# Kernel optimization log

Measured on AMD Instinct MI355X. Metric: run time of the kernel, lower is better.

Reference implementation:

```python
import jax, jax.numpy as jnp
import numpy as np

L = 4      # num_gnn_layers
D = 128    # dim_latent
N = 50000  # nodes
E = 800000 # edges
BN_EPS = 1e-5


def setup_inputs() -> dict:
    key = jax.random.key(0)
    ks = jax.random.split(key, 16)
    w = lambda k: jax.random.normal(k, (L, D, D), jnp.float32) * 0.05
    b = lambda k: jax.random.normal(k, (L, D), jnp.float32) * 0.05
    return {
        "edge_index": jax.random.randint(ks[0], (2, E), 0, N, dtype=jnp.int64),
        "h": jax.random.normal(ks[1], (N, D), jnp.float32),
        "e": jax.random.normal(ks[2], (E, D), jnp.float32),
        "WA": w(ks[3]), "bA": b(ks[4]),
        "WB": w(ks[5]), "bB": b(ks[6]),
        "WC": w(ks[7]), "bC": b(ks[8]),
        "WU": w(ks[9]), "bU": b(ks[10]),
        "WVf": w(ks[11]), "bVf": b(ks[12]),
        "WVb": w(ks[13]), "bVb": b(ks[14]),
        "bnh_g": jnp.ones((L, D), jnp.float32), "bnh_b": jnp.zeros((L, D), jnp.float32),
        "bne_g": jnp.ones((L, D), jnp.float32), "bne_b": jnp.zeros((L, D), jnp.float32),
    }


def _bn(x, g, b):
    # BatchNorm1d, track_running_stats=False -> batch stats, biased variance
    mu = jnp.mean(x, axis=0)
    var = jnp.mean(jnp.square(x - mu), axis=0)
    return (x - mu) * jax.lax.rsqrt(var + BN_EPS) * g + b


def reference(edge_index, h, e,
              WA, bA, WB, bB, WC, bC, WU, bU, WVf, bVf, WVb, bVb,
              bnh_g, bnh_b, bne_g, bne_b):
    n = h.shape[0]
    s0, s1 = edge_index[0], edge_index[1]  # propagate always uses s0 -> s1

    for l in range(L):
        A = h @ WA[l].T + bA[l]
        B = h @ WB[l].T + bB[l]
        C = e @ WC[l].T + bC[l]
        U = h @ WU[l].T + bU[l]
        Vf = h @ WVf[l].T + bVf[l]
        Vb = h @ WVb[l].T + bVb[l]

        def gate(V, gsrc, gdst):
            ne = A[gsrc] + B[gdst] + C                      # [E, D]
            ne = jax.nn.relu(_bn(ne, bne_g[l], bne_b[l])) + e
            sig = jax.nn.sigmoid(ne)
            msg = V[s0] * sig / (sig + 1e-6)                # [E, D]
            agg = jax.ops.segment_sum(msg, s1, num_segments=n)
            return agg, ne

        h_f, e_f = gate(Vf, s0, s1)   # forward gate
        h_b, _ = gate(Vb, s1, s0)     # backward gate (A/B roles swapped only)

        h_new = jax.nn.relu(_bn(h_f + h_b + U, bnh_g[l], bnh_b[l])) + h
        h, e = h_new, e_f             # dropout is identity in eval

    return h, e
```

## Files before the change

kernel.cpp:

```cpp
#include <hip/hip_runtime.h>
#include <hip/hip_bf16.h>

#define N_NODES 50000
#define N_EDGES 800000
#define DIM 128
#define NLAYERS 4
#define BN_EPS 1e-5f
#define ECH 64

typedef unsigned short bf16_t;
typedef __attribute__((ext_vector_type(8))) short bf16x8;
typedef __attribute__((ext_vector_type(4))) float f32x4;

__device__ __forceinline__ float bf2f(bf16_t x) {
    unsigned int u = ((unsigned int)x) << 16;
    return __uint_as_float(u);
}
__device__ __forceinline__ bf16_t f2bf(float f) {
    unsigned int u = __float_as_uint(f);
    unsigned int r = (u + 0x7FFFu + ((u >> 16) & 1u)) >> 16;
    return (bf16_t)r;
}

__global__ __launch_bounds__(128) void node_gemm(
    const float* __restrict__ h,
    const float* __restrict__ WA, const float* __restrict__ bA,
    const float* __restrict__ WB, const float* __restrict__ bB,
    const float* __restrict__ WU, const float* __restrict__ bU,
    const float* __restrict__ WVf, const float* __restrict__ bVf,
    const float* __restrict__ WVb, const float* __restrict__ bVb,
    bf16_t* __restrict__ A, bf16_t* __restrict__ B, bf16_t* __restrict__ U,
    bf16_t* __restrict__ Vf, bf16_t* __restrict__ Vb)
{
    __shared__ float hl[8][DIM];
    const int t = threadIdx.x;
    const long n0 = (long)blockIdx.x * 8;
    #pragma unroll
    for (int i = 0; i < 8; ++i) hl[i][t] = h[(n0 + i) * DIM + t];
    __syncthreads();

    const float* Ws[5] = {WA, WB, WU, WVf, WVb};
    const float* bs[5] = {bA, bB, bU, bVf, bVb};
    float acc[5][8];
    #pragma unroll
    for (int m = 0; m < 5; ++m) {
        float bv = bs[m][t];
        #pragma unroll
        for (int n = 0; n < 8; ++n) acc[m][n] = bv;
    }
    const float4* wr[5];
    #pragma unroll
    for (int m = 0; m < 5; ++m) wr[m] = (const float4*)(Ws[m] + (size_t)t * DIM);

    #pragma unroll 4
    for (int j4 = 0; j4 < DIM / 4; ++j4) {
        float4 h4[8];
        #pragma unroll
        for (int n = 0; n < 8; ++n) h4[n] = ((const float4*)hl[n])[j4];
        #pragma unroll
        for (int m = 0; m < 5; ++m) {
            float4 w = wr[m][j4];
            #pragma unroll
            for (int n = 0; n < 8; ++n)
                acc[m][n] += w.x * h4[n].x + w.y * h4[n].y + w.z * h4[n].z + w.w * h4[n].w;
        }
    }
    bf16_t* Os[5] = {A, B, U, Vf, Vb};
    #pragma unroll
    for (int m = 0; m < 5; ++m)
        #pragma unroll
        for (int n = 0; n < 8; ++n)
            Os[m][(n0 + n) * DIM + t] = f2bf(acc[m][n]);
}

#define EG_TILE 64
#define EG_TILES 5
#define EG_GRID (N_EDGES / (EG_TILE * EG_TILES))

__global__ __launch_bounds__(256) void edge_gemm_mfma(
    const float* __restrict__ e, const float* __restrict__ WC,
    const float* __restrict__ bC, bf16_t* __restrict__ C)
{
    __shared__ __align__(16) char elds[2][EG_TILE * 256];

    const int tid  = threadIdx.x;
    const int lane = tid & 63;
    const int wv   = tid >> 6;
    const int l16  = lane & 15;
    const int lk   = lane >> 4;

    bf16x8 bfrag[2][4];
    float bias[2];
    #pragma unroll
    for (int nt = 0; nt < 2; ++nt) {
        const int n = wv * 32 + nt * 16 + l16;
        bias[nt] = bC[n];
        #pragma unroll
        for (int ks = 0; ks < 4; ++ks) {
            const int k = ks * 32 + lk * 8;
            const float4* wp = (const float4*)(WC + (size_t)n * DIM + k);
            float4 w0 = wp[0], w1 = wp[1];
            union { bf16x8 v; bf16_t s[8]; } u;
            u.s[0] = f2bf(w0.x); u.s[1] = f2bf(w0.y);
            u.s[2] = f2bf(w0.z); u.s[3] = f2bf(w0.w);
            u.s[4] = f2bf(w1.x); u.s[5] = f2bf(w1.y);
            u.s[6] = f2bf(w1.z); u.s[7] = f2bf(w1.w);
            bfrag[nt][ks] = u.v;
        }
    }

    float4 sreg[4][2];
    const long tile0 = (long)blockIdx.x * EG_TILES;

    auto load_tile = [&](long tile) {
        #pragma unroll
        for (int j = 0; j < 4; ++j) {
            const int idx = j * 256 + tid;
            const int row = idx >> 4, cb = idx & 15;
            const float4* gp = (const float4*)(
                e + (size_t)(tile * EG_TILE + row) * DIM + cb * 8);
            sreg[j][0] = gp[0]; sreg[j][1] = gp[1];
        }
    };
    auto write_lds = [&](int buf) {
        #pragma unroll
        for (int j = 0; j < 4; ++j) {
            const int idx = j * 256 + tid;
            const int row = idx >> 4, cb = idx & 15;
            union { bf16x8 v; bf16_t s[8]; } u;
            float4 a = sreg[j][0], b = sreg[j][1];
            u.s[0] = f2bf(a.x); u.s[1] = f2bf(a.y);
            u.s[2] = f2bf(a.z); u.s[3] = f2bf(a.w);
            u.s[4] = f2bf(b.x); u.s[5] = f2bf(b.y);
            u.s[6] = f2bf(b.z); u.s[7] = f2bf(b.w);
            const int off = row * 256 + ((cb * 16) ^ ((row & 7) << 4));
            *(bf16x8*)(&elds[buf][off]) = u.v;
        }
    };

    load_tile(tile0);
    write_lds(0);
    __syncthreads();
    int cur = 0;

    for (int t = 0; t < EG_TILES; ++t) {
        if (t + 1 < EG_TILES) load_tile(tile0 + t + 1);

        f32x4 acc[4][2];
        #pragma unroll
        for (int mt = 0; mt < 4; ++mt)
            #pragma unroll
            for (int nt = 0; nt < 2; ++nt)
                acc[mt][nt] = (f32x4){0.f, 0.f, 0.f, 0.f};

        #pragma unroll
        for (int ks = 0; ks < 4; ++ks) {
            bf16x8 afrag[4];
            #pragma unroll
            for (int mt = 0; mt < 4; ++mt) {
                const int row = mt * 16 + l16;
                const int off = row * 256 +
                    ((ks * 64 + lk * 16) ^ ((row & 7) << 4));
                afrag[mt] = *(const bf16x8*)(&elds[cur][off]);
            }
            #pragma unroll
            for (int mt = 0; mt < 4; ++mt)
                #pragma unroll
                for (int nt = 0; nt < 2; ++nt)
                    acc[mt][nt] = __builtin_amdgcn_mfma_f32_16x16x32_bf16(
                        afrag[mt], bfrag[nt][ks], acc[mt][nt], 0, 0, 0);
        }

        const long e0 = (tile0 + t) * EG_TILE;
        #pragma unroll
        for (int mt = 0; mt < 4; ++mt) {
            const long rbase = e0 + mt * 16 + lk * 4;
            #pragma unroll
            for (int nt = 0; nt < 2; ++nt) {
                const int col = wv * 32 + nt * 16 + l16;
                #pragma unroll
                for (int r = 0; r < 4; ++r)
                    C[(rbase + r) * DIM + col] = f2bf(acc[mt][nt][r] + bias[nt]);
            }
        }

        if (t + 1 < EG_TILES) {
            write_lds(cur ^ 1);
            __syncthreads();
            cur ^= 1;
        }
    }
}

__global__ __launch_bounds__(128) void edge_stats(
    const int* __restrict__ s0, const int* __restrict__ s1,
    const bf16_t* __restrict__ A, const bf16_t* __restrict__ B,
    const bf16_t* __restrict__ C, float* __restrict__ stats)
{
    __shared__ int ls0[ECH], ls1[ECH];
    const int t = threadIdx.x;
    const long k0 = (long)blockIdx.x * ECH;
    if (t < ECH) { ls0[t] = s0[k0 + t]; ls1[t] = s1[k0 + t]; }
    __syncthreads();

    float sf = 0.f, ssf = 0.f, sb = 0.f, ssb = 0.f;
    for (int i = 0; i < ECH; ++i) {
        const long k = k0 + i;
        const long a = ls0[i], b = ls1[i];
        float c  = bf2f(C[k * DIM + t]);
        float a0 = bf2f(A[a * DIM + t]);
        float b1 = bf2f(B[b * DIM + t]);
        float a1 = bf2f(A[b * DIM + t]);
        float b0 = bf2f(B[a * DIM + t]);
        float tf = a0 + b1 + c;
        float tb = a1 + b0 + c;
        sf += tf; ssf += tf * tf;
        sb += tb; ssb += tb * tb;
    }
    atomicAdd(&stats[t], sf);
    atomicAdd(&stats[128 + t], ssf);
    atomicAdd(&stats[256 + t], sb);
    atomicAdd(&stats[384 + t], ssb);
}

__global__ void finalize_edge_stats(float* __restrict__ stats)
{
    const int t = threadIdx.x;
    const float inv = 1.0f / (float)N_EDGES;
    if (t < 128) {
        float mu = stats[t] * inv;
        float var = stats[128 + t] * inv - mu * mu;
        stats[768 + t] = mu;
        stats[896 + t] = rsqrtf(var + BN_EPS);
    } else {
        int d = t - 128;
        float mu = stats[256 + d] * inv;
        float var = stats[384 + d] * inv - mu * mu;
        stats[1024 + d] = mu;
        stats[1152 + d] = rsqrtf(var + BN_EPS);
    }
}

__global__ __launch_bounds__(128) void edge_apply(
    const int* __restrict__ s0, const int* __restrict__ s1,
    const bf16_t* __restrict__ A, const bf16_t* __restrict__ B,
    const bf16_t* __restrict__ C,
    const bf16_t* __restrict__ Vf, const bf16_t* __restrict__ Vb,
    const float* __restrict__ stats,
    const float* __restrict__ gne, const float* __restrict__ bne,
    float* __restrict__ ebuf, float* __restrict__ agg)
{
    __shared__ int ls0[ECH], ls1[ECH];
    const int t = threadIdx.x;
    const long k0 = (long)blockIdx.x * ECH;
    if (t < ECH) { ls0[t] = s0[k0 + t]; ls1[t] = s1[k0 + t]; }
    __syncthreads();

    const float g = gne[t], bb = bne[t];
    const float af = stats[896 + t] * g;
    const float cf = bb - stats[768 + t] * af;
    const float ab = stats[1152 + t] * g;
    const float cb = bb - stats[1024 + t] * ab;

    for (int i = 0; i < ECH; ++i) {
        const long k = k0 + i;
        const long sa = ls0[i], sd = ls1[i];
        float c  = bf2f(C[k * DIM + t]);
        float a0 = bf2f(A[sa * DIM + t]);
        float b1 = bf2f(B[sd * DIM + t]);
        float a1 = bf2f(A[sd * DIM + t]);
        float b0 = bf2f(B[sa * DIM + t]);
        float ek = ebuf[k * DIM + t];

        float nf = fmaxf((a0 + b1 + c) * af + cf, 0.0f) + ek;
        float nb = fmaxf((a1 + b0 + c) * ab + cb, 0.0f) + ek;
        ebuf[k * DIM + t] = nf;

        float sigf = 1.0f / (1.0f + __expf(-nf));
        float sigb = 1.0f / (1.0f + __expf(-nb));
        float wf = sigf / (sigf + 1e-6f);
        float wb = sigb / (sigb + 1e-6f);
        float msg = bf2f(Vf[sa * DIM + t]) * wf + bf2f(Vb[sa * DIM + t]) * wb;
        atomicAdd(&agg[sd * DIM + t], msg);
    }
}

__global__ __launch_bounds__(128) void node_stats(
    const float* __restrict__ agg, const bf16_t* __restrict__ U,
    float* __restrict__ stats)
{
    const int t = threadIdx.x;
    const long n0 = (long)blockIdx.x * 50;
    float s = 0.f, ss = 0.f;
    for (int i = 0; i < 50; ++i) {
        const long n = n0 + i;
        float v = agg[n * DIM + t] + bf2f(U[n * DIM + t]);
        s += v; ss += v * v;
    }
    atomicAdd(&stats[512 + t], s);
    atomicAdd(&stats[640 + t], ss);
}

__global__ void finalize_node_stats(float* __restrict__ stats)
{
    const int t = threadIdx.x;
    const float inv = 1.0f / (float)N_NODES;
    float mu = stats[512 + t] * inv;
    float var = stats[640 + t] * inv - mu * mu;
    stats[1280 + t] = mu;
    stats[1408 + t] = rsqrtf(var + BN_EPS);
}

__global__ __launch_bounds__(256) void node_apply(
    const float* __restrict__ agg, const bf16_t* __restrict__ U,
    const float* __restrict__ stats,
    const float* __restrict__ gh, const float* __restrict__ bh,
    float* __restrict__ hbuf)
{
    const long i = (long)blockIdx.x * 256 + threadIdx.x;
    const int d = (int)(i & (DIM - 1));
    float v = agg[i] + bf2f(U[i]);
    float n = (v - stats[1280 + d]) * stats[1408 + d] * gh[d] + bh[d];
    hbuf[i] = fmaxf(n, 0.0f) + hbuf[i];
}

extern "C" void kernel_launch(void* const* d_in, const int* in_sizes, int n_in,
                              void* d_out, int out_size, void* d_ws, size_t ws_size,
                              hipStream_t stream)
{
    const int* ei = (const int*)d_in[0];
    const int* s0 = ei;
    const int* s1 = ei + N_EDGES;
    const float* h0 = (const float*)d_in[1];
    const float* e0 = (const float*)d_in[2];
    const float* WA = (const float*)d_in[3];  const float* bA = (const float*)d_in[4];
    const float* WB = (const float*)d_in[5];  const float* bB = (const float*)d_in[6];
    const float* WC = (const float*)d_in[7];  const float* bC = (const float*)d_in[8];
    const float* WU = (const float*)d_in[9];  const float* bU = (const float*)d_in[10];
    const float* WVf = (const float*)d_in[11]; const float* bVf = (const float*)d_in[12];
    const float* WVb = (const float*)d_in[13]; const float* bVb = (const float*)d_in[14];
    const float* bnh_g = (const float*)d_in[15]; const float* bnh_b = (const float*)d_in[16];
    const float* bne_g = (const float*)d_in[17]; const float* bne_b = (const float*)d_in[18];

    float* hbuf = (float*)d_out;
    float* ebuf = hbuf + (size_t)N_NODES * DIM;

    float* agg = (float*)d_ws;
    float* stats = agg + (size_t)N_NODES * DIM;
    bf16_t* Abuf  = (bf16_t*)(stats + 2048);
    bf16_t* Bbuf  = Abuf  + (size_t)N_NODES * DIM;
    bf16_t* Ubuf  = Bbuf  + (size_t)N_NODES * DIM;
    bf16_t* Vfbuf = Ubuf  + (size_t)N_NODES * DIM;
    bf16_t* Vbbuf = Vfbuf + (size_t)N_NODES * DIM;
    bf16_t* Cbuf  = Vbbuf + (size_t)N_NODES * DIM;

    hipMemcpyAsync(hbuf, h0, (size_t)N_NODES * DIM * sizeof(float),
                   hipMemcpyDeviceToDevice, stream);
    hipMemcpyAsync(ebuf, e0, (size_t)N_EDGES * DIM * sizeof(float),
                   hipMemcpyDeviceToDevice, stream);

    for (int l = 0; l < NLAYERS; ++l) {
        const size_t wo = (size_t)l * DIM * DIM;
        const size_t bo = (size_t)l * DIM;
        hipMemsetAsync(agg, 0, ((size_t)N_NODES * DIM + 768) * sizeof(float), stream);

        node_gemm<<<N_NODES / 8, 128, 0, stream>>>(
            hbuf, WA + wo, bA + bo, WB + wo, bB + bo, WU + wo, bU + bo,
            WVf + wo, bVf + bo, WVb + wo, bVb + bo,
            Abuf, Bbuf, Ubuf, Vfbuf, Vbbuf);
        edge_gemm_mfma<<<EG_GRID, 256, 0, stream>>>(ebuf, WC + wo, bC + bo, Cbuf);
        edge_stats<<<N_EDGES / ECH, 128, 0, stream>>>(s0, s1, Abuf, Bbuf, Cbuf, stats);
        finalize_edge_stats<<<1, 256, 0, stream>>>(stats);
        edge_apply<<<N_EDGES / ECH, 128, 0, stream>>>(
            s0, s1, Abuf, Bbuf, Cbuf, Vfbuf, Vbbuf, stats,
            bne_g + bo, bne_b + bo, ebuf, agg);
        node_stats<<<N_NODES / 50, 128, 0, stream>>>(agg, Ubuf, stats);
        finalize_node_stats<<<1, 128, 0, stream>>>(stats);
        node_apply<<<(N_NODES * DIM) / 256, 256, 0, stream>>>(
            agg, Ubuf, stats, bnh_g + bo, bnh_b + bo, hbuf);
    }
}
```

Before: 5.499 ms.

## Use MFMA for node GEMM and destination-sorted edge apply with run-merged atomics

Replaces the scalar FP32 node GEMM with a bf16 MFMA kernel that converts h and the weights to bf16 on the fly. It also adds a one-time counting sort of edges by destination (histogram, scan, scatter), so edge_apply walks edges in destination order. Consecutive messages to the same node are then summed in a register before one atomic, and the destination's A/B rows are reused across the run. The cost is extra preprocessing kernels, a single-block scan, and random gathers into C and the edge features through perm instead of streaming reads.

```diff
diff --git a/kernel.cpp b/kernel.cpp
--- a/kernel.cpp
+++ b/kernel.cpp
@@ -22,7 +22,59 @@
     return (bf16_t)r;
 }
 
-__global__ __launch_bounds__(128) void node_gemm(
+__global__ __launch_bounds__(256) void hist_kernel(
+    const int* __restrict__ s1, int* __restrict__ deg)
+{
+    int k = blockIdx.x * 256 + threadIdx.x;
+    if (k < N_EDGES) atomicAdd(&deg[s1[k]], 1);
+}
+
+__global__ __launch_bounds__(1024) void scan_kernel(
+    const int* __restrict__ deg, int* __restrict__ cursor)
+{
+    __shared__ int part[1024];
+    const int t = threadIdx.x;
+    const int CH = (N_NODES + 1023) / 1024;
+    const int base = t * CH;
+    int s = 0;
+    for (int i = 0; i < CH; ++i) {
+        int n = base + i;
+        if (n < N_NODES) s += deg[n];
+    }
+    part[t] = s;
+    __syncthreads();
+    for (int off = 1; off < 1024; off <<= 1) {
+        int v = (t >= off) ? part[t - off] : 0;
+        __syncthreads();
+        part[t] += v;
+        __syncthreads();
+    }
+    int run = part[t] - s;
+    for (int i = 0; i < CH; ++i) {
+        int n = base + i;
+        if (n < N_NODES) { cursor[n] = run; run += deg[n]; }
+    }
+}
+
+__global__ __launch_bounds__(256) void scatter_kernel(
+    const int* __restrict__ s0, const int* __restrict__ s1,
+    int* __restrict__ cursor, int* __restrict__ perm,
+    int* __restrict__ ssrc, int* __restrict__ sdst)
+{
+    int k = blockIdx.x * 256 + threadIdx.x;
+    if (k < N_EDGES) {
+        int d = s1[k];
+        int pos = atomicAdd(&cursor[d], 1);
+        perm[pos] = k;
+        ssrc[pos] = s0[k];
+        sdst[pos] = d;
+    }
+}
+
+#define NG_TILE 64
+#define NG_GRID ((N_NODES + NG_TILE - 1) / NG_TILE)
+
+__global__ __launch_bounds__(256) void node_gemm_mfma(
     const float* __restrict__ h,
     const float* __restrict__ WA, const float* __restrict__ bA,
     const float* __restrict__ WB, const float* __restrict__ bB,
@@ -32,45 +84,100 @@
     bf16_t* __restrict__ A, bf16_t* __restrict__ B, bf16_t* __restrict__ U,
     bf16_t* __restrict__ Vf, bf16_t* __restrict__ Vb)
 {
-    __shared__ float hl[8][DIM];
-    const int t = threadIdx.x;
-    const long n0 = (long)blockIdx.x * 8;
+    __shared__ __align__(16) char hlds[NG_TILE * 256];
+
+    const int tid  = threadIdx.x;
+    const int lane = tid & 63;
+    const int wv   = tid >> 6;
+    const int l16  = lane & 15;
+    const int lk   = lane >> 4;
+    const long n0  = (long)blockIdx.x * NG_TILE;
+
     #pragma unroll
-    for (int i = 0; i < 8; ++i) hl[i][t] = h[(n0 + i) * DIM + t];
+    for (int j = 0; j < 4; ++j) {
+        const int idx = j * 256 + tid;
+        const int row = idx >> 4, cb = idx & 15;
+        long r = n0 + row;
+        if (r >= N_NODES) r = N_NODES - 1;
+        const float4* gp = (const float4*)(h + (size_t)r * DIM + cb * 8);
+        float4 a = gp[0], b = gp[1];
+        union { bf16x8 v; bf16_t s[8]; } u;
+        u.s[0] = f2bf(a.x); u.s[1] = f2bf(a.y);
+        u.s[2] = f2bf(a.z); u.s[3] = f2bf(a.w);
+        u.s[4] = f2bf(b.x); u.s[5] = f2bf(b.y);
+        u.s[6] = f2bf(b.z); u.s[7] = f2bf(b.w);
+        const int off = row * 256 + ((cb * 16) ^ ((row & 7) << 4));
+        *(bf16x8*)(&hlds[off]) = u.v;
+    }
     __syncthreads();
+
+    bf16x8 afrag[4][4];
+    #pragma unroll
+    for (int ks = 0; ks < 4; ++ks)
+        #pragma unroll
+        for (int mt = 0; mt < 4; ++mt) {
+            const int row = mt * 16 + l16;
+            const int off = row * 256 + ((ks * 64 + lk * 16) ^ ((row & 7) << 4));
+            afrag[ks][mt] = *(const bf16x8*)(&hlds[off]);
+        }
 
     const float* Ws[5] = {WA, WB, WU, WVf, WVb};
     const float* bs[5] = {bA, bB, bU, bVf, bVb};
-    float acc[5][8];
+    bf16_t* Os[5] = {A, B, U, Vf, Vb};
+
     #pragma unroll
     for (int m = 0; m < 5; ++m) {
-        float bv = bs[m][t];
-        #pragma unroll
-        for (int n = 0; n < 8; ++n) acc[m][n] = bv;
-    }
-    const float4* wr[5];
-    #pragma unroll
-    for (int m = 0; m < 5; ++m) wr[m] = (const float4*)(Ws[m] + (size_t)t * DIM);
-
-    #pragma unroll 4
-    for (int j4 = 0; j4 < DIM / 4; ++j4) {
-        float4 h4[8];
-        #pragma unroll
-        for (int n = 0; n < 8; ++n) h4[n] = ((const float4*)hl[n])[j4];
-        #pragma unroll
-        for (int m = 0; m < 5; ++m) {
-            float4 w = wr[m][j4];
-            #pragma unroll
-            for (int n = 0; n < 8; ++n)
-                acc[m][n] += w.x * h4[n].x + w.y * h4[n].y + w.z * h4[n].z + w.w * h4[n].w;
-        }
-    }
-    bf16_t* Os[5] = {A, B, U, Vf, Vb};
-    #pragma unroll
-    for (int m = 0; m < 5; ++m)
-        #pragma unroll
-        for (int n = 0; n < 8; ++n)
-            Os[m][(n0 + n) * DIM + t] = f2bf(acc[m][n]);
+        bf16x8 bfrag[2][4];
+        float bias[2];
+        #pragma unroll
+        for (int nt = 0; nt < 2; ++nt) {
+            const int n = wv * 32 + nt * 16 + l16;
+            bias[nt] = bs[m][n];
+            #pragma unroll
+            for (int ks = 0; ks < 4; ++ks) {
+                const int k = ks * 32 + lk * 8;
+                const float4* wp = (const float4*)(Ws[m] + (size_t)n * DIM + k);
+                float4 w0 = wp[0], w1 = wp[1];
+                union { bf16x8 v; bf16_t s[8]; } u;
+                u.s[0] = f2bf(w0.x); u.s[1] = f2bf(w0.y);
+                u.s[2] = f2bf(w0.z); u.s[3] = f2bf(w0.w);
+                u.s[4] = f2bf(w1.x); u.s[5] = f2bf(w1.y);
+                u.s[6] = f2bf(w1.z); u.s[7] = f2bf(w1.w);
+                bfrag[nt][ks] = u.v;
+            }
+        }
+
+        f32x4 acc[4][2];
+        #pragma unroll
+        for (int mt = 0; mt < 4; ++mt)
+            #pragma unroll
+            for (int nt = 0; nt < 2; ++nt)
+                acc[mt][nt] = (f32x4){0.f, 0.f, 0.f, 0.f};
+
+        #pragma unroll
+        for (int ks = 0; ks < 4; ++ks)
+            #pragma unroll
+            for (int mt = 0; mt < 4; ++mt)
+                #pragma unroll
+                for (int nt = 0; nt < 2; ++nt)
+                    acc[mt][nt] = __builtin_amdgcn_mfma_f32_16x16x32_bf16(
+                        afrag[ks][mt], bfrag[nt][ks], acc[mt][nt], 0, 0, 0);
+
+        #pragma unroll
+        for (int mt = 0; mt < 4; ++mt) {
+            const long rbase = n0 + mt * 16 + lk * 4;
+            #pragma unroll
+            for (int nt = 0; nt < 2; ++nt) {
+                const int col = wv * 32 + nt * 16 + l16;
+                #pragma unroll
+                for (int r = 0; r < 4; ++r) {
+                    const long rr = rbase + r;
+                    if (rr < N_NODES)
+                        Os[m][rr * DIM + col] = f2bf(acc[mt][nt][r] + bias[nt]);
+                }
+            }
+        }
+    }
 }
 
 #define EG_TILE 64
@@ -241,8 +348,9 @@
     }
 }
 
-__global__ __launch_bounds__(128) void edge_apply(
-    const int* __restrict__ s0, const int* __restrict__ s1,
+__global__ __launch_bounds__(128) void edge_apply_sorted(
+    const int* __restrict__ perm, const int* __restrict__ ssrc,
+    const int* __restrict__ sdst,
     const bf16_t* __restrict__ A, const bf16_t* __restrict__ B,
     const bf16_t* __restrict__ C,
     const bf16_t* __restrict__ Vf, const bf16_t* __restrict__ Vb,
@@ -250,10 +358,14 @@
     const float* __restrict__ gne, const float* __restrict__ bne,
     float* __restrict__ ebuf, float* __restrict__ agg)
 {
-    __shared__ int ls0[ECH], ls1[ECH];
+    __shared__ int lp[ECH], lsa[ECH], lsd[ECH];
     const int t = threadIdx.x;
-    const long k0 = (long)blockIdx.x * ECH;
-    if (t < ECH) { ls0[t] = s0[k0 + t]; ls1[t] = s1[k0 + t]; }
+    const long p0 = (long)blockIdx.x * ECH;
+    if (t < ECH) {
+        lp[t]  = perm[p0 + t];
+        lsa[t] = ssrc[p0 + t];
+        lsd[t] = sdst[p0 + t];
+    }
     __syncthreads();
 
     const float g = gne[t], bb = bne[t];
@@ -262,27 +374,38 @@
     const float ab = stats[1152 + t] * g;
     const float cb = bb - stats[1024 + t] * ab;
 
+    int cur = lsd[0];
+    float Ad = bf2f(A[(long)cur * DIM + t]);
+    float Bd = bf2f(B[(long)cur * DIM + t]);
+    float acc = 0.f;
+
     for (int i = 0; i < ECH; ++i) {
-        const long k = k0 + i;
-        const long sa = ls0[i], sd = ls1[i];
+        const int sd = lsd[i];
+        if (sd != cur) {
+            atomicAdd(&agg[(long)cur * DIM + t], acc);
+            acc = 0.f;
+            cur = sd;
+            Ad = bf2f(A[(long)cur * DIM + t]);
+            Bd = bf2f(B[(long)cur * DIM + t]);
+        }
+        const long k  = lp[i];
+        const long sa = lsa[i];
         float c  = bf2f(C[k * DIM + t]);
         float a0 = bf2f(A[sa * DIM + t]);
-        float b1 = bf2f(B[sd * DIM + t]);
-        float a1 = bf2f(A[sd * DIM + t]);
         float b0 = bf2f(B[sa * DIM + t]);
         float ek = ebuf[k * DIM + t];
 
-        float nf = fmaxf((a0 + b1 + c) * af + cf, 0.0f) + ek;
-        float nb = fmaxf((a1 + b0 + c) * ab + cb, 0.0f) + ek;
+        float nf = fmaxf((a0 + Bd + c) * af + cf, 0.0f) + ek;
+        float nb = fmaxf((Ad + b0 + c) * ab + cb, 0.0f) + ek;
         ebuf[k * DIM + t] = nf;
 
         float sigf = 1.0f / (1.0f + __expf(-nf));
         float sigb = 1.0f / (1.0f + __expf(-nb));
         float wf = sigf / (sigf + 1e-6f);
         float wb = sigb / (sigb + 1e-6f);
-        float msg = bf2f(Vf[sa * DIM + t]) * wf + bf2f(Vb[sa * DIM + t]) * wb;
-        atomicAdd(&agg[sd * DIM + t], msg);
-    }
+        acc += bf2f(Vf[sa * DIM + t]) * wf + bf2f(Vb[sa * DIM + t]) * wb;
+    }
+    atomicAdd(&agg[(long)cur * DIM + t], acc);
 }
 
 __global__ __launch_bounds__(128) void node_stats(
@@ -353,26 +476,37 @@
     bf16_t* Vfbuf = Ubuf  + (size_t)N_NODES * DIM;
     bf16_t* Vbbuf = Vfbuf + (size_t)N_NODES * DIM;
     bf16_t* Cbuf  = Vbbuf + (size_t)N_NODES * DIM;
+    int* deg    = (int*)(Cbuf + (size_t)N_EDGES * DIM);
+    int* cursor = deg + N_NODES;
+    int* perm   = cursor + N_NODES;
+    int* ssrc   = perm + N_EDGES;
+    int* sdst   = ssrc + N_EDGES;
 
     hipMemcpyAsync(hbuf, h0, (size_t)N_NODES * DIM * sizeof(float),
                    hipMemcpyDeviceToDevice, stream);
     hipMemcpyAsync(ebuf, e0, (size_t)N_EDGES * DIM * sizeof(float),
                    hipMemcpyDeviceToDevice, stream);
 
+    hipMemsetAsync(deg, 0, N_NODES * sizeof(int), stream);
+    hist_kernel<<<(N_EDGES + 255) / 256, 256, 0, stream>>>(s1, deg);
+    scan_kernel<<<1, 1024, 0, stream>>>(deg, cursor);
+    scatter_kernel<<<(N_EDGES + 255) / 256, 256, 0, stream>>>(
+        s0, s1, cursor, perm, ssrc, sdst);
+
     for (int l = 0; l < NLAYERS; ++l) {
         const size_t wo = (size_t)l * DIM * DIM;
         const size_t bo = (size_t)l * DIM;
         hipMemsetAsync(agg, 0, ((size_t)N_NODES * DIM + 768) * sizeof(float), stream);
 
-        node_gemm<<<N_NODES / 8, 128, 0, stream>>>(
+        node_gemm_mfma<<<NG_GRID, 256, 0, stream>>>(
             hbuf, WA + wo, bA + bo, WB + wo, bB + bo, WU + wo, bU + bo,
             WVf + wo, bVf + bo, WVb + wo, bVb + bo,
             Abuf, Bbuf, Ubuf, Vfbuf, Vbbuf);
         edge_gemm_mfma<<<EG_GRID, 256, 0, stream>>>(ebuf, WC + wo, bC + bo, Cbuf);
         edge_stats<<<N_EDGES / ECH, 128, 0, stream>>>(s0, s1, Abuf, Bbuf, Cbuf, stats);
         finalize_edge_stats<<<1, 256, 0, stream>>>(stats);
-        edge_apply<<<N_EDGES / ECH, 128, 0, stream>>>(
-            s0, s1, Abuf, Bbuf, Cbuf, Vfbuf, Vbbuf, stats,
+        edge_apply_sorted<<<N_EDGES / ECH, 128, 0, stream>>>(
+            perm, ssrc, sdst, Abuf, Bbuf, Cbuf, Vfbuf, Vbbuf, stats,
             bne_g + bo, bne_b + bo, ebuf, agg);
         node_stats<<<N_NODES / 50, 128, 0, stream>>>(agg, Ubuf, stats);
         finalize_node_stats<<<1, 128, 0, stream>>>(stats);
```

New measurement: 4.601 ms. 1.2x faster.
